# Kernel optimization log

Hardware: AMD Instinct MI355X
Metric: run time of the kernel (lower is better)

Reference implementation:

```python
import jax, jax.numpy as jnp
import numpy as np

IN_F = 4096
OUT_F = 4096
B, S = 2, 2048


def setup_inputs() -> dict:
    key = jax.random.key(0)
    k1, k2, k3, k4 = jax.random.split(key, 4)
    input = jax.random.normal(k1, (B, S, IN_F), dtype=jnp.float32)
    int8_weights = jax.random.randint(k2, (OUT_F, IN_F), -128, 128, dtype=jnp.int32).astype(jnp.int8)
    scales = jax.random.normal(k3, (OUT_F,), dtype=jnp.float32)
    bias = jax.random.normal(k4, (1, OUT_F), dtype=jnp.float32)
    return {"input": input, "int8_weights": int8_weights, "scales": scales, "bias": bias}


def reference(input, int8_weights, scales, bias):
    # F.linear(x, W) = x @ W.T ; dequant via per-output-channel scale, then bias
    w = int8_weights.astype(input.dtype)          # [out, in]
    out = jnp.einsum('bsi,oi->bso', input, w)     # [B, S, out]
    out = out * scales + bias                      # broadcast [out] and [1, out]
    return out
```

## Files before the change

kernel.cpp:

```cpp
#include <hip/hip_runtime.h>
#include <hip/hip_bf16.h>

typedef unsigned short u16;
typedef unsigned int u32;
typedef unsigned char u8;
typedef __attribute__((ext_vector_type(4))) int i32x4;

#define MM 4096
#define NN 4096
#define KK 4096

#define BAR __builtin_amdgcn_s_barrier()
#define FENCE asm volatile("" ::: "memory")
#define WAITVM(n) asm volatile("s_waitcnt vmcnt(" #n ")" ::: "memory")

#define ABUF(sh, b) ((sh) + (b) * 32768)
#define BBUF(sh, b) ((sh) + 16384 + (b) * 32768)

__global__ __launch_bounds__(256) void cvt_k(const int* __restrict__ w,
                                             u8* __restrict__ ow,
                                             const float* __restrict__ x,
                                             u8* __restrict__ oa,
                                             float* __restrict__ dA) {
  const int bid = blockIdx.x;
  const int t = threadIdx.x;
  if (bid < 4096) {
    int i = bid * 256 + t;
    const int4* w4 = (const int4*)w + (size_t)i * 4;
    i32x4 r;
#pragma unroll
    for (int j = 0; j < 4; ++j) {
      int4 v = w4[j];
      r[j] = (v.x & 255) | ((v.y & 255) << 8) | ((v.z & 255) << 16) |
             ((u32)(v.w & 255) << 24);
    }
    *(i32x4*)(ow + (size_t)i * 16) = r;
  } else {
    const int row = bid - 4096;
    const float4* xr = (const float4*)(x + (size_t)row * KK);
    float4 v[4];
    float mx = 0.f;
#pragma unroll
    for (int j = 0; j < 4; ++j) {
      v[j] = xr[t + j * 256];
      mx = fmaxf(mx, fmaxf(fmaxf(fabsf(v[j].x), fabsf(v[j].y)),
                           fmaxf(fabsf(v[j].z), fabsf(v[j].w))));
    }
#pragma unroll
    for (int off = 32; off; off >>= 1) mx = fmaxf(mx, __shfl_down(mx, off));
    __shared__ float sm[4];
    if ((t & 63) == 0) sm[t >> 6] = mx;
    __syncthreads();
    mx = fmaxf(fmaxf(sm[0], sm[1]), fmaxf(sm[2], sm[3]));
    mx = fmaxf(mx, 1e-20f);
    const float inv = 127.0f / mx;
    if (t == 0) dA[row] = mx / 127.0f;
    u32* orow = (u32*)(oa + (size_t)row * KK);
#pragma unroll
    for (int j = 0; j < 4; ++j) {
      int qx = (int)rintf(v[j].x * inv), qy = (int)rintf(v[j].y * inv);
      int qz = (int)rintf(v[j].z * inv), qw = (int)rintf(v[j].w * inv);
      orow[t + j * 256] =
          (qx & 255) | ((qy & 255) << 8) | ((qz & 255) << 16) | ((u32)(qw & 255) << 24);
    }
  }
}

__device__ __forceinline__ void gload16(const u8* g, u8* l) {
  __builtin_amdgcn_global_load_lds(
      (const __attribute__((address_space(1))) void*)g,
      (__attribute__((address_space(3))) void*)l, 16, 0, 0);
}

__device__ __forceinline__ void stage_half(const u8* __restrict__ gRowBase,
                                           int k0, u8* ldsHalf, int tid) {
  int row = tid >> 2;
  int c = (tid & 3) ^ ((row >> 1) & 3);
  gload16(gRowBase + (size_t)row * KK + k0 + c * 16, ldsHalf + tid * 16);
}

__device__ __forceinline__ i32x4 ldsfrag(const u8* base, int r, int q) {
  return *(const i32x4*)(base + r * 64 + (((q ^ (r >> 1)) & 3) << 4));
}

#define MFMAI8(a, b, c) __builtin_amdgcn_mfma_i32_16x16x64_i8(a, b, c, 0, 0, 0)

template <int MODE>
__device__ __forceinline__ void do_tile(
    int t, i32x4 (&acc)[8][4], const u8* Ag, const u8* Wg, u8* sh,
    int tid, int lr, int hi, int wr, int wc,
    i32x4 (&afr0)[4], i32x4 (&afr1)[4], i32x4 (&bfr01)[2], i32x4 (&bfr23)[2]) {
  const int b = t & 1;
  u8* Acur = ABUF(sh, b);
  u8* Anxt = ABUF(sh, b ^ 1);
  u8* Bcur = BBUF(sh, b);
  u8* Bnxt = BBUF(sh, b ^ 1);

#pragma unroll
  for (int n = 0; n < 2; ++n)
    bfr23[n] = ldsfrag(Bcur, wc * 64 + (2 + n) * 16 + lr, hi);
  __builtin_amdgcn_s_setprio(1);
#pragma unroll
  for (int m = 0; m < 4; ++m)
#pragma unroll
    for (int n = 0; n < 2; ++n)
      acc[m][n] = MFMAI8(afr0[m], bfr01[n], acc[m][n]);
  __builtin_amdgcn_s_setprio(0);
  FENCE; BAR;

#pragma unroll
  for (int m = 0; m < 4; ++m)
    afr1[m] = ldsfrag(Acur, wr * 128 + 64 + m * 16 + lr, hi);
  if (MODE == 0) {
    stage_half(Wg,            (t + 2) * 64, Bcur,        tid);
    stage_half(Wg + 128 * KK, (t + 2) * 64, Bcur + 8192, tid);
  }
  __builtin_amdgcn_s_setprio(1);
#pragma unroll
  for (int m = 0; m < 4; ++m)
#pragma unroll
    for (int n = 0; n < 2; ++n)
      acc[m][2 + n] = MFMAI8(afr0[m], bfr23[n], acc[m][2 + n]);
  __builtin_amdgcn_s_setprio(0);
  if (MODE == 0) { WAITVM(2); } else if (MODE == 1) { WAITVM(0); }
  FENCE; BAR;

  if (MODE <= 1) {
#pragma unroll
    for (int m = 0; m < 4; ++m)
      afr0[m] = ldsfrag(Anxt, wr * 128 + m * 16 + lr, hi);
  }
  if (MODE == 0) {
    stage_half(Ag,            (t + 2) * 64, Acur,        tid);
    stage_half(Ag + 128 * KK, (t + 2) * 64, Acur + 8192, tid);
  }
  __builtin_amdgcn_s_setprio(1);
#pragma unroll
  for (int m = 0; m < 4; ++m)
#pragma unroll
    for (int n = 0; n < 2; ++n)
      acc[4 + m][n] = MFMAI8(afr1[m], bfr01[n], acc[4 + m][n]);
  __builtin_amdgcn_s_setprio(0);

  if (MODE <= 1) {
#pragma unroll
    for (int n = 0; n < 2; ++n)
      bfr01[n] = ldsfrag(Bnxt, wc * 64 + n * 16 + lr, hi);
  }
  __builtin_amdgcn_s_setprio(1);
#pragma unroll
  for (int m = 0; m < 4; ++m)
#pragma unroll
    for (int n = 0; n < 2; ++n)
      acc[4 + m][2 + n] = MFMAI8(afr1[m], bfr23[n], acc[4 + m][2 + n]);
  __builtin_amdgcn_s_setprio(0);
}

__global__ __launch_bounds__(512, 2) void gemm_k(const u8* __restrict__ A,
                                                 const u8* __restrict__ W,
                                                 const float* __restrict__ dA,
                                                 const float* __restrict__ scales,
                                                 const float* __restrict__ bias,
                                                 float* __restrict__ out) {
  __shared__ u8 sh[65536];

  const int cpx = gridDim.x >> 3;
  const int wg = (blockIdx.x & 7) * cpx + (blockIdx.x >> 3);
  const int bm = wg >> 4;
  const int bn = wg & 15;

  const int tid = threadIdx.x;
  const int lane = tid & 63;
  const int lr = lane & 15;
  const int hi = lane >> 4;
  const int wid = tid >> 6;
  const int wr = wid >> 2;
  const int wc = wid & 3;

  i32x4 acc[8][4] = {};
  i32x4 afr0[4], afr1[4], bfr01[2], bfr23[2];

  const u8* Ag = A + (size_t)bm * 256 * KK;
  const u8* Wg = W + (size_t)bn * 256 * KK;

  stage_half(Wg,             0, BBUF(sh, 0),        tid);
  stage_half(Wg + 128 * KK,  0, BBUF(sh, 0) + 8192, tid);
  stage_half(Ag,             0, ABUF(sh, 0),        tid);
  stage_half(Ag + 128 * KK,  0, ABUF(sh, 0) + 8192, tid);
  stage_half(Wg,            64, BBUF(sh, 1),        tid);
  stage_half(Wg + 128 * KK, 64, BBUF(sh, 1) + 8192, tid);
  stage_half(Ag,            64, ABUF(sh, 1),        tid);
  stage_half(Ag + 128 * KK, 64, ABUF(sh, 1) + 8192, tid);
  WAITVM(4);
  BAR;
#pragma unroll
  for (int m = 0; m < 4; ++m)
    afr0[m] = ldsfrag(ABUF(sh, 0), wr * 128 + m * 16 + lr, hi);
#pragma unroll
  for (int n = 0; n < 2; ++n)
    bfr01[n] = ldsfrag(BBUF(sh, 0), wc * 64 + n * 16 + lr, hi);

  for (int t = 0; t < 62; ++t)
    do_tile<0>(t, acc, Ag, Wg, sh, tid, lr, hi, wr, wc, afr0, afr1, bfr01, bfr23);
  do_tile<1>(62, acc, Ag, Wg, sh, tid, lr, hi, wr, wc, afr0, afr1, bfr01, bfr23);
  do_tile<2>(63, acc, Ag, Wg, sh, tid, lr, hi, wr, wc, afr0, afr1, bfr01, bfr23);

  const int colb = bn * 256 + wc * 64 + lr;
  const int rowb0 = bm * 256 + wr * 128 + (hi << 2);
#pragma unroll
  for (int m = 0; m < 8; ++m) {
    const int row = rowb0 + m * 16;
    const float da0 = dA[row], da1 = dA[row + 1], da2 = dA[row + 2], da3 = dA[row + 3];
#pragma unroll
    for (int n = 0; n < 4; ++n) {
      const int col = colb + n * 16;
      const float sc = scales[col];
      const float bi = bias[col];
      out[(size_t)(row + 0) * NN + col] = (float)acc[m][n][0] * (da0 * sc) + bi;
      out[(size_t)(row + 1) * NN + col] = (float)acc[m][n][1] * (da1 * sc) + bi;
      out[(size_t)(row + 2) * NN + col] = (float)acc[m][n][2] * (da2 * sc) + bi;
      out[(size_t)(row + 3) * NN + col] = (float)acc[m][n][3] * (da3 * sc) + bi;
    }
  }
}

__global__ __launch_bounds__(256) void fb_k(const float* __restrict__ A,
                                            const int* __restrict__ W,
                                            const float* __restrict__ scales,
                                            const float* __restrict__ bias,
                                            float* __restrict__ out) {
  __shared__ float Arow[KK];
  const int m = blockIdx.y;
  const int n0 = blockIdx.x * 256;
  const int tid = threadIdx.x;
  for (int k = tid; k < KK; k += 256) Arow[k] = A[(size_t)m * KK + k];
  __syncthreads();
  const int n = n0 + tid;
  float acc = 0.f;
  const int* wrp = W + (size_t)n * KK;
  for (int k = 0; k < KK; ++k) acc += Arow[k] * (float)wrp[k];
  out[(size_t)m * NN + n] = acc * scales[n] + bias[n];
}

extern "C" void kernel_launch(void* const* d_in, const int* in_sizes, int n_in,
                              void* d_out, int out_size, void* d_ws, size_t ws_size,
                              hipStream_t stream) {
  const float* input = (const float*)d_in[0];
  const int* w8 = (const int*)d_in[1];
  const float* scales = (const float*)d_in[2];
  const float* bias = (const float*)d_in[3];
  float* out = (float*)d_out;

  const size_t nelem = (size_t)NN * KK;
  const size_t need = 2 * nelem + MM * sizeof(float);

  if (ws_size >= need) {
    u8* Wq = (u8*)d_ws;
    u8* Aq = Wq + nelem;
    float* dA = (float*)(Aq + nelem);
    cvt_k<<<8192, 256, 0, stream>>>(w8, Wq, input, Aq, dA);
    gemm_k<<<256, 512, 0, stream>>>(Aq, Wq, dA, scales, bias, out);
  } else {
    dim3 grid(NN / 256, MM);
    fb_k<<<grid, 256, 0, stream>>>(input, w8, scales, bias, out);
  }
}
```

Baseline: 95.65 us.

## Load weight fragments directly from global into registers, bypassing LDS staging

After: 123.2 us. +28.8%, slower.

```diff
diff --git a/kernel.cpp b/kernel.cpp
--- a/kernel.cpp
+++ b/kernel.cpp
@@ -14,8 +14,7 @@
 #define FENCE asm volatile("" ::: "memory")
 #define WAITVM(n) asm volatile("s_waitcnt vmcnt(" #n ")" ::: "memory")
 
-#define ABUF(sh, b) ((sh) + (b) * 32768)
-#define BBUF(sh, b) ((sh) + 16384 + (b) * 32768)
+#define ABUF(sh, b) ((sh) + (b) * 16384)
 
 __global__ __launch_bounds__(256) void cvt_k(const int* __restrict__ w,
                                              u8* __restrict__ ow,
@@ -87,72 +86,65 @@
 
 template <int MODE>
 __device__ __forceinline__ void do_tile(
-    int t, i32x4 (&acc)[8][4], const u8* Ag, const u8* Wg, u8* sh,
-    int tid, int lr, int hi, int wr, int wc,
-    i32x4 (&afr0)[4], i32x4 (&afr1)[4], i32x4 (&bfr01)[2], i32x4 (&bfr23)[2]) {
+    int t, i32x4 (&acc)[8][4], const u8* Ag, const u8* Bg, u8* sh,
+    int tid, int lr, int hi, int wr,
+    i32x4 (&afr0)[4], i32x4 (&afr1)[4], i32x4 (&bC)[4], i32x4 (&bN)[4]) {
   const int b = t & 1;
   u8* Acur = ABUF(sh, b);
   u8* Anxt = ABUF(sh, b ^ 1);
-  u8* Bcur = BBUF(sh, b);
-  u8* Bnxt = BBUF(sh, b ^ 1);
-
-#pragma unroll
-  for (int n = 0; n < 2; ++n)
-    bfr23[n] = ldsfrag(Bcur, wc * 64 + (2 + n) * 16 + lr, hi);
-  __builtin_amdgcn_s_setprio(1);
-#pragma unroll
-  for (int m = 0; m < 4; ++m)
-#pragma unroll
-    for (int n = 0; n < 2; ++n)
-      acc[m][n] = MFMAI8(afr0[m], bfr01[n], acc[m][n]);
-  __builtin_amdgcn_s_setprio(0);
-  FENCE; BAR;
+
+  if (MODE <= 1) {
+#pragma unroll
+    for (int n = 0; n < 4; ++n)
+      bN[n] = *(const i32x4*)(Bg + (size_t)n * (16 * KK) + (t + 1) * 64);
+  }
+  if (MODE <= 1) { WAITVM(6); } else { WAITVM(0); }
+  __builtin_amdgcn_s_setprio(1);
+#pragma unroll
+  for (int m = 0; m < 4; ++m)
+#pragma unroll
+    for (int n = 0; n < 2; ++n)
+      acc[m][n] = MFMAI8(afr0[m], bC[n], acc[m][n]);
+  __builtin_amdgcn_s_setprio(0);
 
 #pragma unroll
   for (int m = 0; m < 4; ++m)
     afr1[m] = ldsfrag(Acur, wr * 128 + 64 + m * 16 + lr, hi);
-  if (MODE == 0) {
-    stage_half(Wg,            (t + 2) * 64, Bcur,        tid);
-    stage_half(Wg + 128 * KK, (t + 2) * 64, Bcur + 8192, tid);
-  }
-  __builtin_amdgcn_s_setprio(1);
-#pragma unroll
-  for (int m = 0; m < 4; ++m)
-#pragma unroll
-    for (int n = 0; n < 2; ++n)
-      acc[m][2 + n] = MFMAI8(afr0[m], bfr23[n], acc[m][2 + n]);
-  __builtin_amdgcn_s_setprio(0);
-  if (MODE == 0) { WAITVM(2); } else if (MODE == 1) { WAITVM(0); }
-  FENCE; BAR;
-
+  __builtin_amdgcn_s_setprio(1);
+#pragma unroll
+  for (int m = 0; m < 4; ++m)
+#pragma unroll
+    for (int n = 0; n < 2; ++n)
+      acc[m][2 + n] = MFMAI8(afr0[m], bC[2 + n], acc[m][2 + n]);
+  __builtin_amdgcn_s_setprio(0);
   if (MODE <= 1) {
-#pragma unroll
-    for (int m = 0; m < 4; ++m)
-      afr0[m] = ldsfrag(Anxt, wr * 128 + m * 16 + lr, hi);
-  }
+    WAITVM(4);
+    FENCE; BAR;
+  }
+
   if (MODE == 0) {
     stage_half(Ag,            (t + 2) * 64, Acur,        tid);
     stage_half(Ag + 128 * KK, (t + 2) * 64, Acur + 8192, tid);
   }
-  __builtin_amdgcn_s_setprio(1);
-#pragma unroll
-  for (int m = 0; m < 4; ++m)
-#pragma unroll
-    for (int n = 0; n < 2; ++n)
-      acc[4 + m][n] = MFMAI8(afr1[m], bfr01[n], acc[4 + m][n]);
-  __builtin_amdgcn_s_setprio(0);
-
   if (MODE <= 1) {
 #pragma unroll
-    for (int n = 0; n < 2; ++n)
-      bfr01[n] = ldsfrag(Bnxt, wc * 64 + n * 16 + lr, hi);
-  }
-  __builtin_amdgcn_s_setprio(1);
-#pragma unroll
-  for (int m = 0; m < 4; ++m)
-#pragma unroll
-    for (int n = 0; n < 2; ++n)
-      acc[4 + m][2 + n] = MFMAI8(afr1[m], bfr23[n], acc[4 + m][2 + n]);
+    for (int m = 0; m < 4; ++m)
+      afr0[m] = ldsfrag(Anxt, wr * 128 + m * 16 + lr, hi);
+  }
+  __builtin_amdgcn_s_setprio(1);
+#pragma unroll
+  for (int m = 0; m < 4; ++m)
+#pragma unroll
+    for (int n = 0; n < 2; ++n)
+      acc[4 + m][n] = MFMAI8(afr1[m], bC[n], acc[4 + m][n]);
+  __builtin_amdgcn_s_setprio(0);
+
+  __builtin_amdgcn_s_setprio(1);
+#pragma unroll
+  for (int m = 0; m < 4; ++m)
+#pragma unroll
+    for (int n = 0; n < 2; ++n)
+      acc[4 + m][2 + n] = MFMAI8(afr1[m], bC[2 + n], acc[4 + m][2 + n]);
   __builtin_amdgcn_s_setprio(0);
 }
 
@@ -162,7 +154,7 @@
                                                  const float* __restrict__ scales,
                                                  const float* __restrict__ bias,
                                                  float* __restrict__ out) {
-  __shared__ u8 sh[65536];
+  __shared__ u8 sh[32768];
 
   const int cpx = gridDim.x >> 3;
   const int wg = (blockIdx.x & 7) * cpx + (blockIdx.x >> 3);
@@ -178,32 +170,30 @@
   const int wc = wid & 3;
 
   i32x4 acc[8][4] = {};
-  i32x4 afr0[4], afr1[4], bfr01[2], bfr23[2];
+  i32x4 afr0[4], afr1[4], bE[4], bO[4];
 
   const u8* Ag = A + (size_t)bm * 256 * KK;
-  const u8* Wg = W + (size_t)bn * 256 * KK;
-
-  stage_half(Wg,             0, BBUF(sh, 0),        tid);
-  stage_half(Wg + 128 * KK,  0, BBUF(sh, 0) + 8192, tid);
+  const u8* Bg = W + ((size_t)(bn * 256 + wc * 64 + lr)) * KK + hi * 16;
+
   stage_half(Ag,             0, ABUF(sh, 0),        tid);
   stage_half(Ag + 128 * KK,  0, ABUF(sh, 0) + 8192, tid);
-  stage_half(Wg,            64, BBUF(sh, 1),        tid);
-  stage_half(Wg + 128 * KK, 64, BBUF(sh, 1) + 8192, tid);
+#pragma unroll
+  for (int n = 0; n < 4; ++n)
+    bE[n] = *(const i32x4*)(Bg + (size_t)n * (16 * KK));
   stage_half(Ag,            64, ABUF(sh, 1),        tid);
   stage_half(Ag + 128 * KK, 64, ABUF(sh, 1) + 8192, tid);
-  WAITVM(4);
-  BAR;
+  WAITVM(6);
+  FENCE; BAR;
 #pragma unroll
   for (int m = 0; m < 4; ++m)
     afr0[m] = ldsfrag(ABUF(sh, 0), wr * 128 + m * 16 + lr, hi);
-#pragma unroll
-  for (int n = 0; n < 2; ++n)
-    bfr01[n] = ldsfrag(BBUF(sh, 0), wc * 64 + n * 16 + lr, hi);
-
-  for (int t = 0; t < 62; ++t)
-    do_tile<0>(t, acc, Ag, Wg, sh, tid, lr, hi, wr, wc, afr0, afr1, bfr01, bfr23);
-  do_tile<1>(62, acc, Ag, Wg, sh, tid, lr, hi, wr, wc, afr0, afr1, bfr01, bfr23);
-  do_tile<2>(63, acc, Ag, Wg, sh, tid, lr, hi, wr, wc, afr0, afr1, bfr01, bfr23);
+
+  for (int tt = 0; tt < 31; ++tt) {
+    do_tile<0>(tt * 2,     acc, Ag, Bg, sh, tid, lr, hi, wr, afr0, afr1, bE, bO);
+    do_tile<0>(tt * 2 + 1, acc, Ag, Bg, sh, tid, lr, hi, wr, afr0, afr1, bO, bE);
+  }
+  do_tile<1>(62, acc, Ag, Bg, sh, tid, lr, hi, wr, afr0, afr1, bE, bO);
+  do_tile<2>(63, acc, Ag, Bg, sh, tid, lr, hi, wr, afr0, afr1, bO, bE);
 
   const int colb = bn * 256 + wc * 64 + lr;
   const int rowb0 = bm * 256 + wr * 128 + (hi << 2);
```

## Double the K-tile to 128 and restructure the LDS pipeline with one barrier per tile

Applied to the files above, without the earlier changes.

Measured after the change: 90.28 us, median of 3. 1.06x faster.

```diff
diff --git a/kernel.cpp b/kernel.cpp
--- a/kernel.cpp
+++ b/kernel.cpp
@@ -14,8 +14,8 @@
 #define FENCE asm volatile("" ::: "memory")
 #define WAITVM(n) asm volatile("s_waitcnt vmcnt(" #n ")" ::: "memory")
 
-#define ABUF(sh, b) ((sh) + (b) * 32768)
-#define BBUF(sh, b) ((sh) + 16384 + (b) * 32768)
+#define ABUF(sh, b) ((sh) + (b) * 65536)
+#define BBUF(sh, b) ((sh) + 32768 + (b) * 65536)
 
 __global__ __launch_bounds__(256) void cvt_k(const int* __restrict__ w,
                                              u8* __restrict__ ow,
@@ -72,24 +72,25 @@
       (__attribute__((address_space(3))) void*)l, 16, 0, 0);
 }
 
-__device__ __forceinline__ void stage_half(const u8* __restrict__ gRowBase,
-                                           int k0, u8* ldsHalf, int tid) {
-  int row = tid >> 2;
-  int c = (tid & 3) ^ ((row >> 1) & 3);
-  gload16(gRowBase + (size_t)row * KK + k0 + c * 16, ldsHalf + tid * 16);
+__device__ __forceinline__ void stage_q(const u8* __restrict__ gRowBase,
+                                        int k0, u8* lds, int tid, int pass) {
+  int p = pass * 512 + tid;
+  int row = p >> 3;
+  int c = (p & 7) ^ (row & 7);
+  gload16(gRowBase + (size_t)row * KK + k0 + c * 16, lds + p * 16);
 }
 
 __device__ __forceinline__ i32x4 ldsfrag(const u8* base, int r, int q) {
-  return *(const i32x4*)(base + r * 64 + (((q ^ (r >> 1)) & 3) << 4));
+  return *(const i32x4*)(base + r * 128 + (((q ^ r) & 7) << 4));
 }
 
 #define MFMAI8(a, b, c) __builtin_amdgcn_mfma_i32_16x16x64_i8(a, b, c, 0, 0, 0)
 
-template <int MODE>
+template <bool LAST>
 __device__ __forceinline__ void do_tile(
     int t, i32x4 (&acc)[8][4], const u8* Ag, const u8* Wg, u8* sh,
     int tid, int lr, int hi, int wr, int wc,
-    i32x4 (&afr0)[4], i32x4 (&afr1)[4], i32x4 (&bfr01)[2], i32x4 (&bfr23)[2]) {
+    i32x4 (&afr0)[4], i32x4 (&afr1)[4], i32x4 (&b01)[2], i32x4 (&b23)[2]) {
   const int b = t & 1;
   u8* Acur = ABUF(sh, b);
   u8* Anxt = ABUF(sh, b ^ 1);
@@ -98,61 +99,106 @@
 
 #pragma unroll
   for (int n = 0; n < 2; ++n)
-    bfr23[n] = ldsfrag(Bcur, wc * 64 + (2 + n) * 16 + lr, hi);
-  __builtin_amdgcn_s_setprio(1);
-#pragma unroll
-  for (int m = 0; m < 4; ++m)
-#pragma unroll
-    for (int n = 0; n < 2; ++n)
-      acc[m][n] = MFMAI8(afr0[m], bfr01[n], acc[m][n]);
-  __builtin_amdgcn_s_setprio(0);
-  FENCE; BAR;
+    b23[n] = ldsfrag(Bcur, wc * 64 + (2 + n) * 16 + lr, hi);
+  if (!LAST) {
+#pragma unroll
+    for (int ps = 0; ps < 4; ++ps) stage_q(Wg, (t + 1) * 128, Bnxt, tid, ps);
+  }
+  __builtin_amdgcn_s_setprio(1);
+#pragma unroll
+  for (int m = 0; m < 4; ++m)
+#pragma unroll
+    for (int n = 0; n < 2; ++n)
+      acc[m][n] = MFMAI8(afr0[m], b01[n], acc[m][n]);
+  __builtin_amdgcn_s_setprio(0);
 
 #pragma unroll
   for (int m = 0; m < 4; ++m)
     afr1[m] = ldsfrag(Acur, wr * 128 + 64 + m * 16 + lr, hi);
-  if (MODE == 0) {
-    stage_half(Wg,            (t + 2) * 64, Bcur,        tid);
-    stage_half(Wg + 128 * KK, (t + 2) * 64, Bcur + 8192, tid);
-  }
-  __builtin_amdgcn_s_setprio(1);
-#pragma unroll
-  for (int m = 0; m < 4; ++m)
-#pragma unroll
-    for (int n = 0; n < 2; ++n)
-      acc[m][2 + n] = MFMAI8(afr0[m], bfr23[n], acc[m][2 + n]);
-  __builtin_amdgcn_s_setprio(0);
-  if (MODE == 0) { WAITVM(2); } else if (MODE == 1) { WAITVM(0); }
-  FENCE; BAR;
-
-  if (MODE <= 1) {
+  if (!LAST) {
+#pragma unroll
+    for (int ps = 0; ps < 4; ++ps) stage_q(Ag, (t + 1) * 128, Anxt, tid, ps);
+  }
+  __builtin_amdgcn_s_setprio(1);
+#pragma unroll
+  for (int m = 0; m < 4; ++m)
+#pragma unroll
+    for (int n = 0; n < 2; ++n)
+      acc[m][2 + n] = MFMAI8(afr0[m], b23[n], acc[m][2 + n]);
+  __builtin_amdgcn_s_setprio(0);
+
+#pragma unroll
+  for (int m = 0; m < 4; ++m)
+    afr0[m] = ldsfrag(Acur, wr * 128 + m * 16 + lr, 4 + hi);
+  __builtin_amdgcn_s_setprio(1);
+#pragma unroll
+  for (int m = 0; m < 4; ++m)
+#pragma unroll
+    for (int n = 0; n < 2; ++n)
+      acc[4 + m][n] = MFMAI8(afr1[m], b01[n], acc[4 + m][n]);
+  __builtin_amdgcn_s_setprio(0);
+
+#pragma unroll
+  for (int n = 0; n < 2; ++n)
+    b01[n] = ldsfrag(Bcur, wc * 64 + n * 16 + lr, 4 + hi);
+  __builtin_amdgcn_s_setprio(1);
+#pragma unroll
+  for (int m = 0; m < 4; ++m)
+#pragma unroll
+    for (int n = 0; n < 2; ++n)
+      acc[4 + m][2 + n] = MFMAI8(afr1[m], b23[n], acc[4 + m][2 + n]);
+  __builtin_amdgcn_s_setprio(0);
+
+#pragma unroll
+  for (int n = 0; n < 2; ++n)
+    b23[n] = ldsfrag(Bcur, wc * 64 + (2 + n) * 16 + lr, 4 + hi);
+  __builtin_amdgcn_s_setprio(1);
+#pragma unroll
+  for (int m = 0; m < 4; ++m)
+#pragma unroll
+    for (int n = 0; n < 2; ++n)
+      acc[m][n] = MFMAI8(afr0[m], b01[n], acc[m][n]);
+  __builtin_amdgcn_s_setprio(0);
+
+#pragma unroll
+  for (int m = 0; m < 4; ++m)
+    afr1[m] = ldsfrag(Acur, wr * 128 + 64 + m * 16 + lr, 4 + hi);
+  __builtin_amdgcn_s_setprio(1);
+#pragma unroll
+  for (int m = 0; m < 4; ++m)
+#pragma unroll
+    for (int n = 0; n < 2; ++n)
+      acc[m][2 + n] = MFMAI8(afr0[m], b23[n], acc[m][2 + n]);
+  __builtin_amdgcn_s_setprio(0);
+  if (!LAST) {
+    WAITVM(0);
+    FENCE; BAR;
+  }
+
+  if (!LAST) {
 #pragma unroll
     for (int m = 0; m < 4; ++m)
       afr0[m] = ldsfrag(Anxt, wr * 128 + m * 16 + lr, hi);
   }
-  if (MODE == 0) {
-    stage_half(Ag,            (t + 2) * 64, Acur,        tid);
-    stage_half(Ag + 128 * KK, (t + 2) * 64, Acur + 8192, tid);
-  }
-  __builtin_amdgcn_s_setprio(1);
-#pragma unroll
-  for (int m = 0; m < 4; ++m)
-#pragma unroll
-    for (int n = 0; n < 2; ++n)
-      acc[4 + m][n] = MFMAI8(afr1[m], bfr01[n], acc[4 + m][n]);
-  __builtin_amdgcn_s_setprio(0);
-
-  if (MODE <= 1) {
-#pragma unroll
-    for (int n = 0; n < 2; ++n)
-      bfr01[n] = ldsfrag(Bnxt, wc * 64 + n * 16 + lr, hi);
-  }
-  __builtin_amdgcn_s_setprio(1);
-#pragma unroll
-  for (int m = 0; m < 4; ++m)
-#pragma unroll
-    for (int n = 0; n < 2; ++n)
-      acc[4 + m][2 + n] = MFMAI8(afr1[m], bfr23[n], acc[4 + m][2 + n]);
+  __builtin_amdgcn_s_setprio(1);
+#pragma unroll
+  for (int m = 0; m < 4; ++m)
+#pragma unroll
+    for (int n = 0; n < 2; ++n)
+      acc[4 + m][n] = MFMAI8(afr1[m], b01[n], acc[4 + m][n]);
+  __builtin_amdgcn_s_setprio(0);
+
+  if (!LAST) {
+#pragma unroll
+    for (int n = 0; n < 2; ++n)
+      b01[n] = ldsfrag(Bnxt, wc * 64 + n * 16 + lr, hi);
+  }
+  __builtin_amdgcn_s_setprio(1);
+#pragma unroll
+  for (int m = 0; m < 4; ++m)
+#pragma unroll
+    for (int n = 0; n < 2; ++n)
+      acc[4 + m][2 + n] = MFMAI8(afr1[m], b23[n], acc[4 + m][2 + n]);
   __builtin_amdgcn_s_setprio(0);
 }
 
@@ -162,7 +208,7 @@
                                                  const float* __restrict__ scales,
                                                  const float* __restrict__ bias,
                                                  float* __restrict__ out) {
-  __shared__ u8 sh[65536];
+  __shared__ u8 sh[131072];
 
   const int cpx = gridDim.x >> 3;
   const int wg = (blockIdx.x & 7) * cpx + (blockIdx.x >> 3);
@@ -178,32 +224,27 @@
   const int wc = wid & 3;
 
   i32x4 acc[8][4] = {};
-  i32x4 afr0[4], afr1[4], bfr01[2], bfr23[2];
+  i32x4 afr0[4], afr1[4], b01[2], b23[2];
 
   const u8* Ag = A + (size_t)bm * 256 * KK;
   const u8* Wg = W + (size_t)bn * 256 * KK;
 
-  stage_half(Wg,             0, BBUF(sh, 0),        tid);
-  stage_half(Wg + 128 * KK,  0, BBUF(sh, 0) + 8192, tid);
-  stage_half(Ag,             0, ABUF(sh, 0),        tid);
-  stage_half(Ag + 128 * KK,  0, ABUF(sh, 0) + 8192, tid);
-  stage_half(Wg,            64, BBUF(sh, 1),        tid);
-  stage_half(Wg + 128 * KK, 64, BBUF(sh, 1) + 8192, tid);
-  stage_half(Ag,            64, ABUF(sh, 1),        tid);
-  stage_half(Ag + 128 * KK, 64, ABUF(sh, 1) + 8192, tid);
-  WAITVM(4);
-  BAR;
+#pragma unroll
+  for (int ps = 0; ps < 4; ++ps) stage_q(Wg, 0, BBUF(sh, 0), tid, ps);
+#pragma unroll
+  for (int ps = 0; ps < 4; ++ps) stage_q(Ag, 0, ABUF(sh, 0), tid, ps);
+  WAITVM(0);
+  FENCE; BAR;
 #pragma unroll
   for (int m = 0; m < 4; ++m)
     afr0[m] = ldsfrag(ABUF(sh, 0), wr * 128 + m * 16 + lr, hi);
 #pragma unroll
   for (int n = 0; n < 2; ++n)
-    bfr01[n] = ldsfrag(BBUF(sh, 0), wc * 64 + n * 16 + lr, hi);
-
-  for (int t = 0; t < 62; ++t)
-    do_tile<0>(t, acc, Ag, Wg, sh, tid, lr, hi, wr, wc, afr0, afr1, bfr01, bfr23);
-  do_tile<1>(62, acc, Ag, Wg, sh, tid, lr, hi, wr, wc, afr0, afr1, bfr01, bfr23);
-  do_tile<2>(63, acc, Ag, Wg, sh, tid, lr, hi, wr, wc, afr0, afr1, bfr01, bfr23);
+    b01[n] = ldsfrag(BBUF(sh, 0), wc * 64 + n * 16 + lr, hi);
+
+  for (int t = 0; t < 31; ++t)
+    do_tile<false>(t, acc, Ag, Wg, sh, tid, lr, hi, wr, wc, afr0, afr1, b01, b23);
+  do_tile<true>(31, acc, Ag, Wg, sh, tid, lr, hi, wr, wc, afr0, afr1, b01, b23);
 
   const int colb = bn * 256 + wc * 64 + lr;
   const int rowb0 = bm * 256 + wr * 128 + (hi << 2);
```

## Switch GEMM LDS staging to triple buffering with one barrier per k-tile

Applied to the files above, without the earlier changes.

New measurement: 94.38 us. No clear change (-1.3%).

```diff
diff --git a/kernel.cpp b/kernel.cpp
--- a/kernel.cpp
+++ b/kernel.cpp
@@ -14,8 +14,8 @@
 #define FENCE asm volatile("" ::: "memory")
 #define WAITVM(n) asm volatile("s_waitcnt vmcnt(" #n ")" ::: "memory")
 
-#define ABUF(sh, b) ((sh) + (b) * 32768)
-#define BBUF(sh, b) ((sh) + 16384 + (b) * 32768)
+#define ABUF(sh, i) ((sh) + (i) * 16384)
+#define BBUF(sh, i) ((sh) + 49152 + (i) * 16384)
 
 __global__ __launch_bounds__(256) void cvt_k(const int* __restrict__ w,
                                              u8* __restrict__ ow,
@@ -87,18 +87,19 @@
 
 template <int MODE>
 __device__ __forceinline__ void do_tile(
-    int t, i32x4 (&acc)[8][4], const u8* Ag, const u8* Wg, u8* sh,
-    int tid, int lr, int hi, int wr, int wc,
+    int t, int cur, int nxt, int fut, i32x4 (&acc)[8][4],
+    const u8* Ag, const u8* Wg, u8* sh, int tid, int lr, int hi, int wr, int wc,
     i32x4 (&afr0)[4], i32x4 (&afr1)[4], i32x4 (&bfr01)[2], i32x4 (&bfr23)[2]) {
-  const int b = t & 1;
-  u8* Acur = ABUF(sh, b);
-  u8* Anxt = ABUF(sh, b ^ 1);
-  u8* Bcur = BBUF(sh, b);
-  u8* Bnxt = BBUF(sh, b ^ 1);
+  u8* Acur = ABUF(sh, cur);
+  u8* Bcur = BBUF(sh, cur);
 
 #pragma unroll
   for (int n = 0; n < 2; ++n)
     bfr23[n] = ldsfrag(Bcur, wc * 64 + (2 + n) * 16 + lr, hi);
+  if (MODE == 0) {
+    stage_half(Wg,            (t + 2) * 64, BBUF(sh, fut),        tid);
+    stage_half(Wg + 128 * KK, (t + 2) * 64, BBUF(sh, fut) + 8192, tid);
+  }
   __builtin_amdgcn_s_setprio(1);
 #pragma unroll
   for (int m = 0; m < 4; ++m)
@@ -106,14 +107,13 @@
     for (int n = 0; n < 2; ++n)
       acc[m][n] = MFMAI8(afr0[m], bfr01[n], acc[m][n]);
   __builtin_amdgcn_s_setprio(0);
-  FENCE; BAR;
 
 #pragma unroll
   for (int m = 0; m < 4; ++m)
     afr1[m] = ldsfrag(Acur, wr * 128 + 64 + m * 16 + lr, hi);
   if (MODE == 0) {
-    stage_half(Wg,            (t + 2) * 64, Bcur,        tid);
-    stage_half(Wg + 128 * KK, (t + 2) * 64, Bcur + 8192, tid);
+    stage_half(Ag,            (t + 2) * 64, ABUF(sh, fut),        tid);
+    stage_half(Ag + 128 * KK, (t + 2) * 64, ABUF(sh, fut) + 8192, tid);
   }
   __builtin_amdgcn_s_setprio(1);
 #pragma unroll
@@ -122,38 +122,37 @@
     for (int n = 0; n < 2; ++n)
       acc[m][2 + n] = MFMAI8(afr0[m], bfr23[n], acc[m][2 + n]);
   __builtin_amdgcn_s_setprio(0);
-  if (MODE == 0) { WAITVM(2); } else if (MODE == 1) { WAITVM(0); }
-  FENCE; BAR;
-
+
+  __builtin_amdgcn_s_setprio(1);
+#pragma unroll
+  for (int m = 0; m < 4; ++m)
+#pragma unroll
+    for (int n = 0; n < 2; ++n)
+      acc[4 + m][n] = MFMAI8(afr1[m], bfr01[n], acc[4 + m][n]);
+  __builtin_amdgcn_s_setprio(0);
+
+  __builtin_amdgcn_s_setprio(1);
+#pragma unroll
+  for (int m = 0; m < 4; ++m)
+#pragma unroll
+    for (int n = 0; n < 2; ++n)
+      acc[4 + m][2 + n] = MFMAI8(afr1[m], bfr23[n], acc[4 + m][2 + n]);
+  __builtin_amdgcn_s_setprio(0);
+  if (MODE == 0) {
+    WAITVM(4);
+    FENCE; BAR;
+  } else if (MODE == 1) {
+    WAITVM(0);
+    FENCE; BAR;
+  }
   if (MODE <= 1) {
 #pragma unroll
     for (int m = 0; m < 4; ++m)
-      afr0[m] = ldsfrag(Anxt, wr * 128 + m * 16 + lr, hi);
-  }
-  if (MODE == 0) {
-    stage_half(Ag,            (t + 2) * 64, Acur,        tid);
-    stage_half(Ag + 128 * KK, (t + 2) * 64, Acur + 8192, tid);
-  }
-  __builtin_amdgcn_s_setprio(1);
-#pragma unroll
-  for (int m = 0; m < 4; ++m)
-#pragma unroll
-    for (int n = 0; n < 2; ++n)
-      acc[4 + m][n] = MFMAI8(afr1[m], bfr01[n], acc[4 + m][n]);
-  __builtin_amdgcn_s_setprio(0);
-
-  if (MODE <= 1) {
-#pragma unroll
-    for (int n = 0; n < 2; ++n)
-      bfr01[n] = ldsfrag(Bnxt, wc * 64 + n * 16 + lr, hi);
-  }
-  __builtin_amdgcn_s_setprio(1);
-#pragma unroll
-  for (int m = 0; m < 4; ++m)
-#pragma unroll
-    for (int n = 0; n < 2; ++n)
-      acc[4 + m][2 + n] = MFMAI8(afr1[m], bfr23[n], acc[4 + m][2 + n]);
-  __builtin_amdgcn_s_setprio(0);
+      afr0[m] = ldsfrag(ABUF(sh, nxt), wr * 128 + m * 16 + lr, hi);
+#pragma unroll
+    for (int n = 0; n < 2; ++n)
+      bfr01[n] = ldsfrag(BBUF(sh, nxt), wc * 64 + n * 16 + lr, hi);
+  }
 }
 
 __global__ __launch_bounds__(512, 2) void gemm_k(const u8* __restrict__ A,
@@ -162,7 +161,7 @@
                                                  const float* __restrict__ scales,
                                                  const float* __restrict__ bias,
                                                  float* __restrict__ out) {
-  __shared__ u8 sh[65536];
+  __shared__ u8 sh[98304];
 
   const int cpx = gridDim.x >> 3;
   const int wg = (blockIdx.x & 7) * cpx + (blockIdx.x >> 3);
@@ -192,7 +191,7 @@
   stage_half(Ag,            64, ABUF(sh, 1),        tid);
   stage_half(Ag + 128 * KK, 64, ABUF(sh, 1) + 8192, tid);
   WAITVM(4);
-  BAR;
+  FENCE; BAR;
 #pragma unroll
   for (int m = 0; m < 4; ++m)
     afr0[m] = ldsfrag(ABUF(sh, 0), wr * 128 + m * 16 + lr, hi);
@@ -200,10 +199,18 @@
   for (int n = 0; n < 2; ++n)
     bfr01[n] = ldsfrag(BBUF(sh, 0), wc * 64 + n * 16 + lr, hi);
 
-  for (int t = 0; t < 62; ++t)
-    do_tile<0>(t, acc, Ag, Wg, sh, tid, lr, hi, wr, wc, afr0, afr1, bfr01, bfr23);
-  do_tile<1>(62, acc, Ag, Wg, sh, tid, lr, hi, wr, wc, afr0, afr1, bfr01, bfr23);
-  do_tile<2>(63, acc, Ag, Wg, sh, tid, lr, hi, wr, wc, afr0, afr1, bfr01, bfr23);
+  int cur = 0;
+  for (int t = 0; t < 62; ++t) {
+    const int nxt = (cur + 1 == 3) ? 0 : cur + 1;
+    const int fut = (nxt + 1 == 3) ? 0 : nxt + 1;
+    do_tile<0>(t, cur, nxt, fut, acc, Ag, Wg, sh, tid, lr, hi, wr, wc,
+               afr0, afr1, bfr01, bfr23);
+    cur = nxt;
+  }
+  do_tile<1>(62, 2, 0, 1, acc, Ag, Wg, sh, tid, lr, hi, wr, wc,
+             afr0, afr1, bfr01, bfr23);
+  do_tile<2>(63, 0, 1, 2, acc, Ag, Wg, sh, tid, lr, hi, wr, wc,
+             afr0, afr1, bfr01, bfr23);
 
   const int colb = bn * 256 + wc * 64 + lr;
   const int rowb0 = bm * 256 + wr * 128 + (hi << 2);
```
